# Kernel tuning notes

Measured on AMD Instinct MI355X. Metric: run time of the kernel, lower is better.

The kernel has to match this reference:

```python
import jax, jax.numpy as jnp
import numpy as np

C = 768      # token feature dim
N = 196      # tokens per stream
R_DIM = 2 * 2 * N  # 784 = concat(A row, A col)


def setup_inputs() -> dict:
    key = jax.random.key(0)
    ks = jax.random.split(key, 16)
    s = 1.0 / np.sqrt(C)
    inp = {
        "x": jax.random.normal(ks[0], (128, N, C), dtype=jnp.float32),
        "y": jax.random.normal(ks[1], (128, N, C), dtype=jnp.float32),
        # linear_conv_1: 1x1 conv (768->768) + BN affine (eval) + ReLU
        "W1": jax.random.normal(ks[2], (C, C), dtype=jnp.float32) * s,
        "b1": jnp.zeros((C,), dtype=jnp.float32),
        "g1": jax.random.uniform(ks[3], (C,), dtype=jnp.float32, minval=0.5, maxval=1.5),
        "be1": jax.random.normal(ks[4], (C,), dtype=jnp.float32) * 0.1,
        # linear_conv_2
        "W2": jax.random.normal(ks[5], (C, C), dtype=jnp.float32) * s,
        "b2": jnp.zeros((C,), dtype=jnp.float32),
        "g2": jax.random.uniform(ks[6], (C,), dtype=jnp.float32, minval=0.5, maxval=1.5),
        "be2": jax.random.normal(ks[7], (C,), dtype=jnp.float32) * 0.1,
        # linear_conv_3: 768->768
        "W3": jax.random.normal(ks[8], (C, C), dtype=jnp.float32) * s,
        "b3": jnp.zeros((C,), dtype=jnp.float32),
        # linear_conv_4: 784->784 over relation rows
        "W4": jax.random.normal(ks[9], (784, 784), dtype=jnp.float32) / np.sqrt(784.0),
        "b4": jnp.zeros((784,), dtype=jnp.float32),
        # linear_conv_5: (768+784)->1
        "W5": jax.random.normal(ks[10], (C + 784, 1), dtype=jnp.float32) / np.sqrt(C + 784.0),
        "b5": jnp.zeros((1,), dtype=jnp.float32),
    }
    return inp


def reference(x, y, W1, b1, g1, be1, W2, b2, g2, be2, W3, b3, W4, b4, W5, b5):
    # per-token 1x1 conv + BN(eval)->affine + ReLU
    phi_x = jax.nn.relu((x @ W1 + b1) * g1 + be1)          # [B,196,768]
    phi_y = jax.nn.relu((y @ W2 + b2) * g2 + be2)          # [B,196,768]
    cat_phi = jnp.concatenate([phi_x, phi_y], axis=1)      # [B,392,768]
    # affinity matrix A = cat_phi @ cat_phi^T
    A = jnp.einsum("bnd,bmd->bnm", cat_phi, cat_phi)       # [B,392,392]
    # R[i] = concat(A[i,:], A[:,i]) -> vectorized as [A | A^T]
    R = jnp.concatenate([A, jnp.swapaxes(A, 1, 2)], axis=2)  # [B,392,784]
    v = cat_phi @ W3 + b3                                   # [B,392,768]
    v_ = R @ W4 + b4                                        # [B,392,784]
    cat_v = jnp.concatenate([v, v_], axis=2)                # [B,392,1552]
    W = cat_v @ W5 + b5                                     # [B,392,1]
    # per-token reweighting then sum of the two streams
    out = x * W[:, :N, :] + y * W[:, N:, :]                 # [B,196,768]
    return out
```

## Files before the change

### kernel.cpp

```cpp
#include <hip/hip_runtime.h>

typedef __bf16 bf16_t;
typedef bf16_t bf16x8 __attribute__((ext_vector_type(8)));
typedef float f32x4 __attribute__((ext_vector_type(4)));
typedef float f32x16 __attribute__((ext_vector_type(16)));
typedef unsigned short u16x8 __attribute__((ext_vector_type(8)));
typedef unsigned short u16x4 __attribute__((ext_vector_type(4)));

#define CD 768
#define NT 196
#define NB 128
#define T2 392
#define MROWS (NB*NT)
#define NTILE 1176

__device__ __forceinline__ unsigned short f2bf(float f){
  unsigned u = __float_as_uint(f);
  u += 0x7fffu + ((u >> 16) & 1u);
  return (unsigned short)(u >> 16);
}
__device__ __forceinline__ float bf2f(unsigned short h){
  return __uint_as_float(((unsigned)h) << 16);
}
__device__ __forceinline__ float wave_reduce(float v){
  #pragma unroll
  for (int o = 32; o > 0; o >>= 1) v += __shfl_down(v, o, 64);
  return v;
}
__device__ __forceinline__ void gload16(const void* g, void* l){
  __builtin_amdgcn_global_load_lds(
      (const __attribute__((address_space(1))) unsigned int*)g,
      (__attribute__((address_space(3))) unsigned int*)l, 16, 0, 0);
}

__global__ __launch_bounds__(256) void prep_pack(const float* __restrict__ W1,
                        const float* __restrict__ W2,
                        unsigned short* __restrict__ W1p, unsigned short* __restrict__ W2p){
  __shared__ float tile[64][33];
  const float* src = blockIdx.z ? W2 : W1;
  unsigned short* dst = blockIdx.z ? W2p : W1p;
  const int kt = blockIdx.x, g = blockIdx.y, tid = threadIdx.x;
  #pragma unroll
  for (int e = 0; e < 8; ++e){
    int idx = e*256 + tid;
    int kk = idx >> 5, nn = idx & 31;
    tile[kk][nn] = src[(size_t)(kt*64 + kk)*CD + g*32 + nn];
  }
  __syncthreads();
  const int ks = tid >> 6, lane = tid & 63;
  const int l31 = lane & 31, lh = lane >> 5;
  unsigned short* o = dst + ((size_t)((g*12 + kt)*4 + ks)*64 + lane)*8;
  #pragma unroll
  for (int i = 0; i < 8; ++i)
    o[i] = f2bf(tile[ks*16 + lh*8 + i][l31]);
}

__global__ void prep_u(const float* __restrict__ W3, const float* __restrict__ W4,
                       const float* __restrict__ W5, const float* __restrict__ b3,
                       const float* __restrict__ b4, const float* __restrict__ b5,
                       float* __restrict__ u3, float* __restrict__ u4s, float* __restrict__ cbuf){
  int wid = (blockIdx.x*blockDim.x + threadIdx.x) >> 6;
  int lane = threadIdx.x & 63;
  const float* w5a = W5;
  const float* w5b = W5 + CD;
  float s = 0.f;
  if (wid < CD){
    const float* row = W3 + (size_t)wid*CD;
    for (int k = lane; k < CD; k += 64) s += row[k]*w5a[k];
    s = wave_reduce(s);
    if (lane == 0) u3[wid] = s;
  } else if (wid < CD + T2){
    int j = wid - CD;
    const float* r0 = W4 + (size_t)j*784;
    const float* r1 = W4 + (size_t)(j+T2)*784;
    for (int e = lane; e < 784; e += 64) s += (r0[e]+r1[e])*w5b[e];
    s = wave_reduce(s);
    if (lane == 0) u4s[j] = s;
  } else if (wid == CD + T2){
    for (int k = lane; k < CD; k += 64) s += b3[k]*w5a[k];
    for (int e = lane; e < 784; e += 64) s += b4[e]*w5b[e];
    s = wave_reduce(s);
    if (lane == 0) cbuf[0] = s + b5[0];
  }
}

__global__ void init_t(const float* __restrict__ u3, float* __restrict__ t){
  int i = blockIdx.x*256 + threadIdx.x;
  if (i < (NB+2)*CD) t[i] = (i < NB*CD) ? u3[i % CD] : 0.f;
}

__global__ __launch_bounds__(256) void cvt2(const float* __restrict__ x,
                                            const float* __restrict__ y,
                                            unsigned short* __restrict__ dst){
  const int nv = MROWS*CD/8;
  for (int id = blockIdx.x*256 + threadIdx.x; id < 2*nv; id += gridDim.x*256){
    const float* s = (id < nv) ? x : y;
    int i = (id < nv) ? id : id - nv;
    float4 a = ((const float4*)s)[i*2];
    float4 b = ((const float4*)s)[i*2+1];
    u16x8 o = { f2bf(a.x), f2bf(a.y), f2bf(a.z), f2bf(a.w),
                f2bf(b.x), f2bf(b.y), f2bf(b.z), f2bf(b.w) };
    ((u16x8*)dst)[id] = o;
  }
}

__global__ __launch_bounds__(256, 4) void phi_gemm2(
    const unsigned short* __restrict__ Ax, const unsigned short* __restrict__ Ay,
    const unsigned short* __restrict__ W1p, const unsigned short* __restrict__ W2p,
    const float* __restrict__ biasX, const float* __restrict__ gamX, const float* __restrict__ betX,
    const float* __restrict__ biasY, const float* __restrict__ gamY, const float* __restrict__ betY,
    const float* __restrict__ u4s,
    unsigned short* __restrict__ Px, unsigned short* __restrict__ Py,
    float* __restrict__ t, int mode)
{
  __shared__ unsigned short As[2][128*64];

  const int tid  = threadIdx.x;
  const int lane = tid & 63;
  const int w    = tid >> 6;
  const int wr = w >> 1, wc = w & 1;

  const int chunk = gridDim.x >> 3;
  int orig = blockIdx.x;
  int swz  = (orig & 7)*chunk + (orig >> 3);
  int s, r;
  if (mode < 0){ s = swz >= NTILE; r = swz - s*NTILE; }
  else         { s = mode; r = swz; }
  const int bn = r % 6;
  const int bm = r / 6;

  const unsigned short* A  = s ? Ay : Ax;
  const unsigned short* Wp = s ? W2p : W1p;
  const float* bias = s ? biasY : biasX;
  const float* gam  = s ? gamY  : gamX;
  const float* bet  = s ? betY  : betX;
  const float* u4c  = u4s + s*NT;
  unsigned short* phi = s ? Py : Px;

  const int srow = lane >> 3;
  const int p    = lane & 7;
  const int g0   = (p - srow) & 7;
  const unsigned short* aB = A + (size_t)(bm*128 + w*32 + srow)*CD + g0*8;

  const unsigned short* bb0 = Wp + ((size_t)(bn*4 + wc*2    )*48)*512 + lane*8;
  const unsigned short* bb1 = Wp + ((size_t)(bn*4 + wc*2 + 1)*48)*512 + lane*8;

  const int l31 = lane & 31;
  const int lh  = lane >> 5;
  const int r7  = l31 & 7;

  f32x16 acc[2][2] = {};

#define STAGE(D, KT) { const int _ko = (KT)*64;                        \
    _Pragma("unroll")                                                  \
    for (int cc = 0; cc < 4; ++cc)                                     \
      gload16(aB + (size_t)cc*8*CD + _ko, &As[D][w*2048 + cc*512]); }

  STAGE(0, 0)
  __syncthreads();

  #pragma unroll 1
  for (int kt = 0; kt < 12; ++kt){
    const int D = kt & 1;
    bf16x8 bq0[4], bq1[4];
    #pragma unroll
    for (int ks = 0; ks < 4; ++ks){
      bq0[ks] = *(const bf16x8*)(bb0 + (kt*4 + ks)*512);
      bq1[ks] = *(const bf16x8*)(bb1 + (kt*4 + ks)*512);
    }
    if (kt < 11) STAGE(D^1, kt+1)
    #pragma unroll
    for (int ks = 0; ks < 4; ++ks){
      const int phys = ((ks*2 + lh) + r7) & 7;
      bf16x8 af0 = *(const bf16x8*)(&As[D][(wr*64      + l31)*64 + phys*8]);
      bf16x8 af1 = *(const bf16x8*)(&As[D][(wr*64 + 32 + l31)*64 + phys*8]);
      acc[0][0] = __builtin_amdgcn_mfma_f32_32x32x16_bf16(af0, bq0[ks], acc[0][0], 0, 0, 0);
      acc[0][1] = __builtin_amdgcn_mfma_f32_32x32x16_bf16(af0, bq1[ks], acc[0][1], 0, 0, 0);
      acc[1][0] = __builtin_amdgcn_mfma_f32_32x32x16_bf16(af1, bq0[ks], acc[1][0], 0, 0, 0);
      acc[1][1] = __builtin_amdgcn_mfma_f32_32x32x16_bf16(af1, bq1[ks], acc[1][1], 0, 0, 0);
    }
    if (kt < 11) __syncthreads();
  }
#undef STAGE

  const int b_base = (bm*128) / NT;
  int  col0 = bn*128 + wc*64 + l31;
  float bi0 = bias[col0],    ga0 = gam[col0],    be0 = bet[col0];
  float bi1 = bias[col0+32], ga1 = gam[col0+32], be1 = bet[col0+32];
  float cb[2][2] = {{0.f,0.f},{0.f,0.f}};
  #pragma unroll
  for (int mi = 0; mi < 2; ++mi){
    #pragma unroll
    for (int reg = 0; reg < 16; ++reg){
      int rg  = bm*128 + wr*64 + mi*32 + (reg & 3) + 8*(reg >> 2) + 4*lh;
      int b   = rg / NT;
      int tok = rg - b*NT;
      float uw = u4c[tok];
      int bk  = b - b_base;
      #pragma unroll
      for (int nj = 0; nj < 2; ++nj){
        float v = (nj ? (acc[mi][nj][reg] + bi1)*ga1 + be1
                      : (acc[mi][nj][reg] + bi0)*ga0 + be0);
        v = fmaxf(v, 0.f);
        phi[(size_t)rg*CD + col0 + nj*32] = f2bf(v);
        float pv = uw*v;
        cb[nj][0] += (bk == 0) ? pv : 0.f;
        cb[nj][1] += (bk == 1) ? pv : 0.f;
      }
    }
  }
  #pragma unroll
  for (int nj = 0; nj < 2; ++nj){
    cb[nj][0] += __shfl_xor(cb[nj][0], 32, 64);
    cb[nj][1] += __shfl_xor(cb[nj][1], 32, 64);
  }
  if (lane < 32){
    atomicAdd(&t[(size_t)(b_base  )*CD + col0   ], cb[0][0]);
    atomicAdd(&t[(size_t)(b_base+1)*CD + col0   ], cb[0][1]);
    atomicAdd(&t[(size_t)(b_base  )*CD + col0+32], cb[1][0]);
    atomicAdd(&t[(size_t)(b_base+1)*CD + col0+32], cb[1][1]);
  }
}

template<bool USEBF>
__global__ __launch_bounds__(256) void comp_wout(
    const unsigned short* __restrict__ phiX, const unsigned short* __restrict__ phiY,
    const float* __restrict__ t, const float* __restrict__ cbuf,
    const float* __restrict__ x, const float* __restrict__ y,
    const unsigned short* __restrict__ xb, const unsigned short* __restrict__ yb,
    float* __restrict__ out)
{
  int gw   = (blockIdx.x*256 + threadIdx.x) >> 6;
  int lane = threadIdx.x & 63;
  int b = gw / NT;
  const unsigned short* px = phiX + (size_t)gw*CD;
  const unsigned short* py = phiY + (size_t)gw*CD;
  const float* tb = t + (size_t)b*CD;
  float s1 = 0.f, s2 = 0.f;
  #pragma unroll
  for (int it = 0; it < 3; ++it){
    int k = it*256 + lane*4;
    float4 tv = *(const float4*)(tb + k);
    u16x4 ux = *(const u16x4*)(px + k);
    u16x4 uy = *(const u16x4*)(py + k);
    s1 += bf2f(ux.x)*tv.x + bf2f(ux.y)*tv.y + bf2f(ux.z)*tv.z + bf2f(ux.w)*tv.w;
    s2 += bf2f(uy.x)*tv.x + bf2f(uy.y)*tv.y + bf2f(uy.z)*tv.z + bf2f(uy.w)*tv.w;
  }
  s1 = wave_reduce(s1);
  s2 = wave_reduce(s2);
  float cc = cbuf[0];
  float wx = __shfl(s1, 0, 64) + cc;
  float wy = __shfl(s2, 0, 64) + cc;
  float* orow = out + (size_t)gw*CD;
  #pragma unroll
  for (int it = 0; it < 3; ++it){
    int k = it*256 + lane*4;
    float4 xv, yv;
    if (USEBF){
      u16x4 a  = *(const u16x4*)(xb + (size_t)gw*CD + k);
      u16x4 c4 = *(const u16x4*)(yb + (size_t)gw*CD + k);
      xv = float4{bf2f(a.x), bf2f(a.y), bf2f(a.z), bf2f(a.w)};
      yv = float4{bf2f(c4.x), bf2f(c4.y), bf2f(c4.z), bf2f(c4.w)};
    } else {
      xv = *(const float4*)(x + (size_t)gw*CD + k);
      yv = *(const float4*)(y + (size_t)gw*CD + k);
    }
    float4 o;
    o.x = xv.x*wx + yv.x*wy;
    o.y = xv.y*wx + yv.y*wy;
    o.z = xv.z*wx + yv.z*wy;
    o.w = xv.w*wx + yv.w*wy;
    *(float4*)(orow + k) = o;
  }
}

extern "C" void kernel_launch(void* const* d_in, const int* in_sizes, int n_in,
                              void* d_out, int out_size, void* d_ws, size_t ws_size,
                              hipStream_t stream){
  const float* x  = (const float*)d_in[0];
  const float* y  = (const float*)d_in[1];
  const float* W1 = (const float*)d_in[2];
  const float* b1 = (const float*)d_in[3];
  const float* g1 = (const float*)d_in[4];
  const float* be1= (const float*)d_in[5];
  const float* W2 = (const float*)d_in[6];
  const float* b2 = (const float*)d_in[7];
  const float* g2 = (const float*)d_in[8];
  const float* be2= (const float*)d_in[9];
  const float* W3 = (const float*)d_in[10];
  const float* b3 = (const float*)d_in[11];
  const float* W4 = (const float*)d_in[12];
  const float* b4 = (const float*)d_in[13];
  const float* W5 = (const float*)d_in[14];
  const float* b5 = (const float*)d_in[15];
  float* out = (float*)d_out;

  const size_t BIGE = (size_t)MROWS*CD;
  const size_t smallF = CD + T2 + 4 + (size_t)(NB+2)*CD;
  const size_t need4 = (2*(size_t)CD*CD + 4*BIGE)*2 + smallF*4 + 256;
  const bool big = (ws_size >= need4);

  unsigned short* W1p = (unsigned short*)d_ws;
  unsigned short* W2p = W1p + CD*CD;
  unsigned short* Sx  = W2p + CD*CD;
  unsigned short* Sy  = Sx + BIGE;
  unsigned short* Px, * Py;
  float* smalls;
  if (big){
    Px = Sy + BIGE;
    Py = Px + BIGE;
    smalls = (float*)(Py + BIGE);
  } else {
    Px = Sy + BIGE;
    Py = Sx;
    smalls = (float*)(Px + BIGE);
  }
  float* u3   = smalls;
  float* u4s  = u3 + CD;
  float* cbuf = u4s + T2;
  float* t    = cbuf + 4;

  prep_pack<<<dim3(12,24,2), 256, 0, stream>>>(W1, W2, W1p, W2p);
  prep_u<<<(CD + T2 + 4)/4, 256, 0, stream>>>(W3, W4, W5, b3, b4, b5, u3, u4s, cbuf);
  init_t<<<((NB+2)*CD + 255)/256, 256, 0, stream>>>(u3, t);

  cvt2<<<2048, 256, 0, stream>>>(x, y, Sx);

  if (big){
    phi_gemm2<<<2*NTILE, 256, 0, stream>>>(Sx, Sy, W1p, W2p,
        b1, g1, be1, b2, g2, be2, u4s, Px, Py, t, -1);
    comp_wout<true><<<MROWS/4, 256, 0, stream>>>(Px, Py, t, cbuf, x, y, Sx, Sy, out);
  } else {
    phi_gemm2<<<NTILE, 256, 0, stream>>>(Sx, Sy, W1p, W2p,
        b1, g1, be1, b2, g2, be2, u4s, Px, Py, t, 0);
    phi_gemm2<<<NTILE, 256, 0, stream>>>(Sx, Sy, W1p, W2p,
        b1, g1, be1, b2, g2, be2, u4s, Px, Py, t, 1);
    comp_wout<false><<<MROWS/4, 256, 0, stream>>>(Px, Py, t, cbuf, x, y, Sx, Sy, out);
  }
}
```

Baseline: 183.8 us.

## Process three N-tiles per block and drop double-buffered A staging

Each phi GEMM block now computes three consecutive 128-column output tiles for the same 128-row A block, so the grid shrinks to a third. The A-tile LDS layout changes to a pre-swizzled MFMA-fragment order with a single buffer and two barriers per k-step, replacing the double-buffered prefetch. The epilogue batch/token split is simplified to a compare instead of a division. This aims to cut block launch overhead and improve L2 locality for A, but gives up load/compute overlap and reduces parallelism, and A is still reloaded from global memory for each of the three tiles.

```diff
diff --git a/kernel.cpp b/kernel.cpp
--- a/kernel.cpp
+++ b/kernel.cpp
@@ -113,21 +113,21 @@
     unsigned short* __restrict__ Px, unsigned short* __restrict__ Py,
     float* __restrict__ t, int mode)
 {
-  __shared__ unsigned short As[2][128*64];
+  __shared__ unsigned short As[16*512];
 
   const int tid  = threadIdx.x;
   const int lane = tid & 63;
   const int w    = tid >> 6;
   const int wr = w >> 1, wc = w & 1;
+  const int l31 = lane & 31, lh = lane >> 5;
 
   const int chunk = gridDim.x >> 3;
-  int orig = blockIdx.x;
-  int swz  = (orig & 7)*chunk + (orig >> 3);
-  int s, r;
-  if (mode < 0){ s = swz >= NTILE; r = swz - s*NTILE; }
-  else         { s = mode; r = swz; }
-  const int bn = r % 6;
-  const int bm = r / 6;
+  const int swz   = (blockIdx.x & 7)*chunk + (blockIdx.x >> 3);
+  const int tile0 = (mode < 0 ? 0 : mode*NTILE) + swz*3;
+  const int s  = tile0 >= NTILE;
+  const int r0 = tile0 - s*NTILE;
+  const int bm  = r0 / 6;
+  const int bn0 = r0 % 6;
 
   const unsigned short* A  = s ? Ay : Ax;
   const unsigned short* Wp = s ? W2p : W1p;
@@ -137,88 +137,72 @@
   const float* u4c  = u4s + s*NT;
   unsigned short* phi = s ? Py : Px;
 
-  const int srow = lane >> 3;
-  const int p    = lane & 7;
-  const int g0   = (p - srow) & 7;
-  const unsigned short* aB = A + (size_t)(bm*128 + w*32 + srow)*CD + g0*8;
-
-  const unsigned short* bb0 = Wp + ((size_t)(bn*4 + wc*2    )*48)*512 + lane*8;
-  const unsigned short* bb1 = Wp + ((size_t)(bn*4 + wc*2 + 1)*48)*512 + lane*8;
-
-  const int l31 = lane & 31;
-  const int lh  = lane >> 5;
-  const int r7  = l31 & 7;
-
-  f32x16 acc[2][2] = {};
-
-#define STAGE(D, KT) { const int _ko = (KT)*64;                        \
-    _Pragma("unroll")                                                  \
-    for (int cc = 0; cc < 4; ++cc)                                     \
-      gload16(aB + (size_t)cc*8*CD + _ko, &As[D][w*2048 + cc*512]); }
-
-  STAGE(0, 0)
-  __syncthreads();
+  const unsigned short* aL = A + (size_t)(bm*128 + l31)*CD + lh*8;
+
+  const int b_base = (bm*128) / NT;
+  const int tokb   = bm*128 - b_base*NT;
 
   #pragma unroll 1
-  for (int kt = 0; kt < 12; ++kt){
-    const int D = kt & 1;
-    bf16x8 bq0[4], bq1[4];
+  for (int j = 0; j < 3; ++j){
+    const int bn = bn0 + j;
+    const unsigned short* bb0 = Wp + ((size_t)(bn*4 + wc*2    )*48)*512 + lane*8;
+    const unsigned short* bb1 = Wp + ((size_t)(bn*4 + wc*2 + 1)*48)*512 + lane*8;
+
+    f32x16 acc[2][2] = {};
+
+    #pragma unroll 1
+    for (int kt = 0; kt < 12; ++kt){
+      #pragma unroll
+      for (int c = 0; c < 4; ++c)
+        gload16(aL + (size_t)c*32*CD + kt*64 + w*16, &As[(c*4 + w)*512]);
+      __syncthreads();
+      #pragma unroll
+      for (int ks = 0; ks < 4; ++ks){
+        bf16x8 bq0 = *(const bf16x8*)(bb0 + (kt*4 + ks)*512);
+        bf16x8 bq1 = *(const bf16x8*)(bb1 + (kt*4 + ks)*512);
+        bf16x8 af0 = *(const bf16x8*)(&As[((wr*2    )*4 + ks)*512 + lane*8]);
+        bf16x8 af1 = *(const bf16x8*)(&As[((wr*2 + 1)*4 + ks)*512 + lane*8]);
+        acc[0][0] = __builtin_amdgcn_mfma_f32_32x32x16_bf16(af0, bq0, acc[0][0], 0, 0, 0);
+        acc[0][1] = __builtin_amdgcn_mfma_f32_32x32x16_bf16(af0, bq1, acc[0][1], 0, 0, 0);
+        acc[1][0] = __builtin_amdgcn_mfma_f32_32x32x16_bf16(af1, bq0, acc[1][0], 0, 0, 0);
+        acc[1][1] = __builtin_amdgcn_mfma_f32_32x32x16_bf16(af1, bq1, acc[1][1], 0, 0, 0);
+      }
+      __syncthreads();
+    }
+
+    int  col0 = bn*128 + wc*64 + l31;
+    float bi0 = bias[col0],    ga0 = gam[col0],    be0 = bet[col0];
+    float bi1 = bias[col0+32], ga1 = gam[col0+32], be1 = bet[col0+32];
+    float cb00 = 0.f, cb01 = 0.f, cb10 = 0.f, cb11 = 0.f;
     #pragma unroll
-    for (int ks = 0; ks < 4; ++ks){
-      bq0[ks] = *(const bf16x8*)(bb0 + (kt*4 + ks)*512);
-      bq1[ks] = *(const bf16x8*)(bb1 + (kt*4 + ks)*512);
-    }
-    if (kt < 11) STAGE(D^1, kt+1)
-    #pragma unroll
-    for (int ks = 0; ks < 4; ++ks){
-      const int phys = ((ks*2 + lh) + r7) & 7;
-      bf16x8 af0 = *(const bf16x8*)(&As[D][(wr*64      + l31)*64 + phys*8]);
-      bf16x8 af1 = *(const bf16x8*)(&As[D][(wr*64 + 32 + l31)*64 + phys*8]);
-      acc[0][0] = __builtin_amdgcn_mfma_f32_32x32x16_bf16(af0, bq0[ks], acc[0][0], 0, 0, 0);
-      acc[0][1] = __builtin_amdgcn_mfma_f32_32x32x16_bf16(af0, bq1[ks], acc[0][1], 0, 0, 0);
-      acc[1][0] = __builtin_amdgcn_mfma_f32_32x32x16_bf16(af1, bq0[ks], acc[1][0], 0, 0, 0);
-      acc[1][1] = __builtin_amdgcn_mfma_f32_32x32x16_bf16(af1, bq1[ks], acc[1][1], 0, 0, 0);
-    }
-    if (kt < 11) __syncthreads();
-  }
-#undef STAGE
-
-  const int b_base = (bm*128) / NT;
-  int  col0 = bn*128 + wc*64 + l31;
-  float bi0 = bias[col0],    ga0 = gam[col0],    be0 = bet[col0];
-  float bi1 = bias[col0+32], ga1 = gam[col0+32], be1 = bet[col0+32];
-  float cb[2][2] = {{0.f,0.f},{0.f,0.f}};
-  #pragma unroll
-  for (int mi = 0; mi < 2; ++mi){
-    #pragma unroll
-    for (int reg = 0; reg < 16; ++reg){
-      int rg  = bm*128 + wr*64 + mi*32 + (reg & 3) + 8*(reg >> 2) + 4*lh;
-      int b   = rg / NT;
-      int tok = rg - b*NT;
-      float uw = u4c[tok];
-      int bk  = b - b_base;
+    for (int mi = 0; mi < 2; ++mi){
       #pragma unroll
-      for (int nj = 0; nj < 2; ++nj){
-        float v = (nj ? (acc[mi][nj][reg] + bi1)*ga1 + be1
-                      : (acc[mi][nj][reg] + bi0)*ga0 + be0);
-        v = fmaxf(v, 0.f);
-        phi[(size_t)rg*CD + col0 + nj*32] = f2bf(v);
-        float pv = uw*v;
-        cb[nj][0] += (bk == 0) ? pv : 0.f;
-        cb[nj][1] += (bk == 1) ? pv : 0.f;
+      for (int reg = 0; reg < 16; ++reg){
+        int roff = wr*64 + mi*32 + (reg & 3) + 8*(reg >> 2) + 4*lh;
+        int tok0 = tokb + roff;
+        int bk   = tok0 >= NT;
+        int tok  = tok0 - (bk ? NT : 0);
+        float uw = u4c[tok];
+        int rg   = bm*128 + roff;
+        float v0 = fmaxf((acc[mi][0][reg] + bi0)*ga0 + be0, 0.f);
+        float v1 = fmaxf((acc[mi][1][reg] + bi1)*ga1 + be1, 0.f);
+        phi[(size_t)rg*CD + col0     ] = f2bf(v0);
+        phi[(size_t)rg*CD + col0 + 32] = f2bf(v1);
+        float p0 = uw*v0, p1 = uw*v1;
+        cb00 += bk ? 0.f : p0;  cb01 += bk ? p0 : 0.f;
+        cb10 += bk ? 0.f : p1;  cb11 += bk ? p1 : 0.f;
       }
     }
-  }
-  #pragma unroll
-  for (int nj = 0; nj < 2; ++nj){
-    cb[nj][0] += __shfl_xor(cb[nj][0], 32, 64);
-    cb[nj][1] += __shfl_xor(cb[nj][1], 32, 64);
-  }
-  if (lane < 32){
-    atomicAdd(&t[(size_t)(b_base  )*CD + col0   ], cb[0][0]);
-    atomicAdd(&t[(size_t)(b_base+1)*CD + col0   ], cb[0][1]);
-    atomicAdd(&t[(size_t)(b_base  )*CD + col0+32], cb[1][0]);
-    atomicAdd(&t[(size_t)(b_base+1)*CD + col0+32], cb[1][1]);
+    cb00 += __shfl_xor(cb00, 32, 64);
+    cb01 += __shfl_xor(cb01, 32, 64);
+    cb10 += __shfl_xor(cb10, 32, 64);
+    cb11 += __shfl_xor(cb11, 32, 64);
+    if (lane < 32){
+      atomicAdd(&t[(size_t)(b_base  )*CD + col0   ], cb00);
+      atomicAdd(&t[(size_t)(b_base+1)*CD + col0   ], cb01);
+      atomicAdd(&t[(size_t)(b_base  )*CD + col0+32], cb10);
+      atomicAdd(&t[(size_t)(b_base+1)*CD + col0+32], cb11);
+    }
   }
 }
 
@@ -327,13 +311,13 @@
   cvt2<<<2048, 256, 0, stream>>>(x, y, Sx);
 
   if (big){
-    phi_gemm2<<<2*NTILE, 256, 0, stream>>>(Sx, Sy, W1p, W2p,
+    phi_gemm2<<<784, 256, 0, stream>>>(Sx, Sy, W1p, W2p,
         b1, g1, be1, b2, g2, be2, u4s, Px, Py, t, -1);
     comp_wout<true><<<MROWS/4, 256, 0, stream>>>(Px, Py, t, cbuf, x, y, Sx, Sy, out);
   } else {
-    phi_gemm2<<<NTILE, 256, 0, stream>>>(Sx, Sy, W1p, W2p,
+    phi_gemm2<<<392, 256, 0, stream>>>(Sx, Sy, W1p, W2p,
         b1, g1, be1, b2, g2, be2, u4s, Px, Py, t, 0);
-    phi_gemm2<<<NTILE, 256, 0, stream>>>(Sx, Sy, W1p, W2p,
+    phi_gemm2<<<392, 256, 0, stream>>>(Sx, Sy, W1p, W2p,
         b1, g1, be1, b2, g2, be2, u4s, Px, Py, t, 1);
     comp_wout<false><<<MROWS/4, 256, 0, stream>>>(Px, Py, t, cbuf, x, y, Sx, Sy, out);
   }
```

Result: slower. 286.4 us (+55.8%).

## Warp-specialize phi GEMM with producer load waves and triple-buffered LDS

Applied to the files above, without the earlier changes.

Doubles the phi_gemm2 block to 512 threads. Four producer waves issue the global-to-LDS loads for A tiles two k-steps ahead into a three-deep LDS ring, while four consumer waves run the MFMA loop at raised priority and load the B fragments directly from global memory. The aim is to overlap A-tile loads with matrix math and cut per-wave load latency stalls. In exchange, half the waves do no math, LDS use per block grows by half, and launch_bounds(512,4) squeezes the register budget, which may cause spills or lower occupancy.

```diff
diff --git a/kernel.cpp b/kernel.cpp
--- a/kernel.cpp
+++ b/kernel.cpp
@@ -27,7 +27,7 @@
   for (int o = 32; o > 0; o >>= 1) v += __shfl_down(v, o, 64);
   return v;
 }
-__device__ __forceinline__ void gload16(const void* g, void* l){
+__device__ __forceinline__ void gload16(const unsigned short* g, unsigned short* l){
   __builtin_amdgcn_global_load_lds(
       (const __attribute__((address_space(1))) unsigned int*)g,
       (__attribute__((address_space(3))) unsigned int*)l, 16, 0, 0);
@@ -104,7 +104,7 @@
   }
 }
 
-__global__ __launch_bounds__(256, 4) void phi_gemm2(
+__global__ __launch_bounds__(512, 4) void phi_gemm2(
     const unsigned short* __restrict__ Ax, const unsigned short* __restrict__ Ay,
     const unsigned short* __restrict__ W1p, const unsigned short* __restrict__ W2p,
     const float* __restrict__ biasX, const float* __restrict__ gamX, const float* __restrict__ betX,
@@ -113,12 +113,15 @@
     unsigned short* __restrict__ Px, unsigned short* __restrict__ Py,
     float* __restrict__ t, int mode)
 {
-  __shared__ unsigned short As[2][128*64];
+  __shared__ unsigned short As[3][128*64];
 
   const int tid  = threadIdx.x;
   const int lane = tid & 63;
   const int w    = tid >> 6;
-  const int wr = w >> 1, wc = w & 1;
+  const bool producer = (w < 4);
+  const int pw = w;
+  const int cw = w & 3;
+  const int wr = cw >> 1, wc = cw & 1;
 
   const int chunk = gridDim.x >> 3;
   int orig = blockIdx.x;
@@ -140,7 +143,7 @@
   const int srow = lane >> 3;
   const int p    = lane & 7;
   const int g0   = (p - srow) & 7;
-  const unsigned short* aB = A + (size_t)(bm*128 + w*32 + srow)*CD + g0*8;
+  const unsigned short* a0 = A + (size_t)(bm*128 + pw*32 + srow)*CD + g0*8;
 
   const unsigned short* bb0 = Wp + ((size_t)(bn*4 + wc*2    )*48)*512 + lane*8;
   const unsigned short* bb1 = Wp + ((size_t)(bn*4 + wc*2 + 1)*48)*512 + lane*8;
@@ -151,37 +154,50 @@
 
   f32x16 acc[2][2] = {};
 
-#define STAGE(D, KT) { const int _ko = (KT)*64;                        \
+#define STAGE(D, KT) { const int ko = (KT)*64;                         \
     _Pragma("unroll")                                                  \
-    for (int cc = 0; cc < 4; ++cc)                                     \
-      gload16(aB + (size_t)cc*8*CD + _ko, &As[D][w*2048 + cc*512]); }
-
-  STAGE(0, 0)
-  __syncthreads();
+    for (int c = 0; c < 4; ++c)                                        \
+      gload16(a0 + (size_t)c*8*CD + ko, &As[D][pw*2048 + c*512]); }
+
+  if (producer){
+    STAGE(0, 0)
+    STAGE(1, 1)
+    asm volatile("s_waitcnt vmcnt(4)" ::: "memory");
+  }
+  __builtin_amdgcn_s_barrier();
 
   #pragma unroll 1
   for (int kt = 0; kt < 12; ++kt){
-    const int D = kt & 1;
-    bf16x8 bq0[4], bq1[4];
-    #pragma unroll
-    for (int ks = 0; ks < 4; ++ks){
-      bq0[ks] = *(const bf16x8*)(bb0 + (kt*4 + ks)*512);
-      bq1[ks] = *(const bf16x8*)(bb1 + (kt*4 + ks)*512);
+    const int D = kt % 3;
+    if (producer){
+      if (kt < 10){
+        STAGE((kt+2) % 3, kt+2)
+        asm volatile("s_waitcnt vmcnt(4)" ::: "memory");
+      } else if (kt == 10){
+        asm volatile("s_waitcnt vmcnt(0)" ::: "memory");
+      }
+    } else {
+      const unsigned short* cA = As[D];
+      __builtin_amdgcn_s_setprio(1);
+      #pragma unroll
+      for (int ks = 0; ks < 4; ++ks){
+        bf16x8 bq0 = *(const bf16x8*)(bb0 + (kt*4 + ks)*512);
+        bf16x8 bq1 = *(const bf16x8*)(bb1 + (kt*4 + ks)*512);
+        const int phys = ((ks*2 + lh) + r7) & 7;
+        bf16x8 af0 = *(const bf16x8*)(&cA[(wr*64      + l31)*64 + phys*8]);
+        bf16x8 af1 = *(const bf16x8*)(&cA[(wr*64 + 32 + l31)*64 + phys*8]);
+        acc[0][0] = __builtin_amdgcn_mfma_f32_32x32x16_bf16(af0, bq0, acc[0][0], 0, 0, 0);
+        acc[0][1] = __builtin_amdgcn_mfma_f32_32x32x16_bf16(af0, bq1, acc[0][1], 0, 0, 0);
+        acc[1][0] = __builtin_amdgcn_mfma_f32_32x32x16_bf16(af1, bq0, acc[1][0], 0, 0, 0);
+        acc[1][1] = __builtin_amdgcn_mfma_f32_32x32x16_bf16(af1, bq1, acc[1][1], 0, 0, 0);
+      }
+      __builtin_amdgcn_s_setprio(0);
     }
-    if (kt < 11) STAGE(D^1, kt+1)
-    #pragma unroll
-    for (int ks = 0; ks < 4; ++ks){
-      const int phys = ((ks*2 + lh) + r7) & 7;
-      bf16x8 af0 = *(const bf16x8*)(&As[D][(wr*64      + l31)*64 + phys*8]);
-      bf16x8 af1 = *(const bf16x8*)(&As[D][(wr*64 + 32 + l31)*64 + phys*8]);
-      acc[0][0] = __builtin_amdgcn_mfma_f32_32x32x16_bf16(af0, bq0[ks], acc[0][0], 0, 0, 0);
-      acc[0][1] = __builtin_amdgcn_mfma_f32_32x32x16_bf16(af0, bq1[ks], acc[0][1], 0, 0, 0);
-      acc[1][0] = __builtin_amdgcn_mfma_f32_32x32x16_bf16(af1, bq0[ks], acc[1][0], 0, 0, 0);
-      acc[1][1] = __builtin_amdgcn_mfma_f32_32x32x16_bf16(af1, bq1[ks], acc[1][1], 0, 0, 0);
-    }
-    if (kt < 11) __syncthreads();
+    __builtin_amdgcn_s_barrier();
   }
 #undef STAGE
+
+  if (producer) return;
 
   const int b_base = (bm*128) / NT;
   int  col0 = bn*128 + wc*64 + l31;
@@ -327,13 +343,13 @@
   cvt2<<<2048, 256, 0, stream>>>(x, y, Sx);
 
   if (big){
-    phi_gemm2<<<2*NTILE, 256, 0, stream>>>(Sx, Sy, W1p, W2p,
+    phi_gemm2<<<2*NTILE, 512, 0, stream>>>(Sx, Sy, W1p, W2p,
         b1, g1, be1, b2, g2, be2, u4s, Px, Py, t, -1);
     comp_wout<true><<<MROWS/4, 256, 0, stream>>>(Px, Py, t, cbuf, x, y, Sx, Sy, out);
   } else {
-    phi_gemm2<<<NTILE, 256, 0, stream>>>(Sx, Sy, W1p, W2p,
+    phi_gemm2<<<NTILE, 512, 0, stream>>>(Sx, Sy, W1p, W2p,
         b1, g1, be1, b2, g2, be2, u4s, Px, Py, t, 0);
-    phi_gemm2<<<NTILE, 256, 0, stream>>>(Sx, Sy, W1p, W2p,
+    phi_gemm2<<<NTILE, 512, 0, stream>>>(Sx, Sy, W1p, W2p,
         b1, g1, be1, b2, g2, be2, u4s, Px, Py, t, 1);
     comp_wout<false><<<MROWS/4, 256, 0, stream>>>(Px, Py, t, cbuf, x, y, Sx, Sy, out);
   }
```

Result: slower. 197.7 us (+7.6%).
